# Performance work log

Measured on AMD Instinct MI355X. Metric: run time of the kernel, lower is better.

## Reference

```python
import math
import jax, jax.numpy as jnp
import numpy as np
from jax import lax

G_RATIO = 0.5       # g_ratio init arg
TMAX_RATIO = 0.25


def setup_inputs() -> dict:
    key = jax.random.key(0)
    k1, k2, k3, k4 = jax.random.split(key, 4)
    N = 4096
    cost_maps = jax.random.uniform(k1, (N,), jnp.float32)          # heuristic h(v)
    nodes = jax.random.uniform(k2, (N, 2), jnp.float32)            # coords (only size used)
    adj = (jax.random.uniform(k3, (N, N)) < 0.005).astype(jnp.float32)
    adj = jnp.maximum(adj, adj.T)                                  # symmetric PRM-like graph
    w = jax.random.uniform(k4, (N, N), jnp.float32, minval=0.1, maxval=1.0)
    weighted_adj = adj * w                                         # edge lengths
    return {"start_index": 0, "goal_index": N - 1, "cost_maps": cost_maps,
            "nodes": nodes, "adj": adj, "weighted_adj": weighted_adj}


def _astar_forward(start_index, goal_index, cost_maps, adj, weighted_adj):
    N = cost_maps.shape[0]
    inv_sqrt_n = 1.0 / math.sqrt(N)
    diag = jnp.arange(N)
    adj = adj.at[diag, diag].set(0.0)
    weighted_adj = jnp.where(jnp.isinf(weighted_adj), 0.0, weighted_adj)
    weighted_adj = weighted_adj.at[diag, diag].set(0.0)

    h = cost_maps
    goal_maps = jnp.zeros((N,), cost_maps.dtype).at[goal_index].set(1.0)
    open0 = jnp.zeros((N,), cost_maps.dtype).at[start_index].set(1.0)
    hist0 = jnp.zeros((N,), cost_maps.dtype)
    g0 = weighted_adj[start_index]
    parents0 = jnp.full((N,), float(goal_index), cost_maps.dtype)
    Tmax = int(TMAX_RATIO * N)  # training-mode budget

    def step(carry, t):
        open_m, hist, g, parents, done, t_final = carry
        f = G_RATIO * g + (1.0 - G_RATIO) * h
        f_exp = jnp.exp(-f * inv_sqrt_n) * open_m
        denom = jnp.sum(f_exp)
        y = f_exp / jnp.where(denom == 0.0, 1.0, denom)  # guard only hits after done
        ind = jnp.argmax(y)
        y_hard = jnp.zeros_like(y).at[ind].set(1.0)
        snm = lax.stop_gradient(y_hard - y) + y  # straight-through one-hot select
        solved = jnp.sum(snm * goal_maps) >= 1e-8
        open2 = jnp.clip(open_m - snm, 0.0, 1.0)
        hist2 = jnp.clip(hist + snm, 0.0, 1.0)
        neighbor = (snm @ adj) * (1.0 - open2) * (1.0 - hist2)   # row-gather via matvec
        g2 = g[ind] + weighted_adj[ind]                          # tentative g through ind
        idx = lax.stop_gradient(((1.0 - open2) * (1.0 - hist2) + open2 * (g > g2).astype(g.dtype)) * neighbor)
        g_new = lax.stop_gradient(g2 * idx + g * (1.0 - idx))
        open3 = lax.stop_gradient(jnp.clip(open2 + idx, 0.0, 1.0))
        parents_new = ind.astype(parents.dtype) * idx + parents * (1.0 - idx)
        keep = done  # freeze state after goal found (mimics torch break)
        carry_out = (jnp.where(keep, open_m, open3),
                     jnp.where(keep, hist, hist2),
                     jnp.where(keep, g, g_new),
                     jnp.where(keep, parents, parents_new),
                     done | solved,
                     jnp.where(keep, t_final, t))
        return carry_out, None

    init = (open0, hist0, g0, parents0, jnp.array(False), jnp.int32(0))
    (open_m, hist, g, parents, done, t_final), _ = lax.scan(
        step, init, jnp.arange(Tmax, dtype=jnp.int32))

    # backtrack: path_maps[loc]=1; loc=parents[loc], repeated t_final times
    parents_i = parents.astype(jnp.int32)
    path0 = goal_maps.astype(jnp.int32)
    loc0 = parents_i[goal_index]

    def bt(carry, i):
        path, loc = carry
        do = i < t_final
        path = jnp.where(do, path.at[loc].set(1), path)
        loc = jnp.where(do, parents_i[loc], loc)
        return (path, loc), None

    (path_maps, _), _ = lax.scan(bt, (path0, loc0), jnp.arange(Tmax, dtype=jnp.int32))
    return hist, path_maps


def reference(start_index, goal_index, cost_maps, nodes, adj, weighted_adj):
    # training-mode forward: returns (histories, path_maps)
    return _astar_forward(start_index, goal_index, cost_maps, adj, weighted_adj)
```

## Files before the change

### kernel.cpp

```cpp
#include <hip/hip_runtime.h>
#include <math.h>


#define NN    4096
#define TMAXI 1024
#define CAP   96
#define STR9  96

__device__ __forceinline__ float fexp_of(float g, float h, float open) {
    float f = __fadd_rn(__fmul_rn(0.5f, g), __fmul_rn(0.5f, h));
    return __fmul_rn(expf(__fmul_rn(-f, 0.015625f)), open);
}

template <int CTRL, int RMASK>
__device__ __forceinline__ double dpp_mov_d(double x) {
    int lo = __double2loint(x), hi = __double2hiint(x);
    lo = __builtin_amdgcn_update_dpp(lo, lo, CTRL, RMASK, 0xf, false);
    hi = __builtin_amdgcn_update_dpp(hi, hi, CTRL, RMASK, 0xf, false);
    return __hiloint2double(hi, lo);
}

__device__ __forceinline__ double wave_max_f64(double x) {
    x = fmax(x, dpp_mov_d<0x111, 0xf>(x));
    x = fmax(x, dpp_mov_d<0x112, 0xf>(x));
    x = fmax(x, dpp_mov_d<0x114, 0xf>(x));
    x = fmax(x, dpp_mov_d<0x118, 0xf>(x));
    x = fmax(x, dpp_mov_d<0x142, 0xa>(x));
    x = fmax(x, dpp_mov_d<0x143, 0xc>(x));
    int lo = __builtin_amdgcn_readlane(__double2loint(x), 63);
    int hi = __builtin_amdgcn_readlane(__double2hiint(x), 63);
    return __hiloint2double(hi, lo);
}

__global__ __launch_bounds__(256)
void build_csr9(const float* __restrict__ wadj, float2* __restrict__ ent)
{
    __shared__ int lcnt;
    const int r = blockIdx.x;
    if (threadIdx.x == 0) lcnt = 0;
    __syncthreads();
    const float4* wrow = (const float4*)(wadj + (size_t)r * NN);
    for (int c = 0; c < NN / (256 * 4); ++c) {
        int t4 = c * 256 + threadIdx.x;
        float4 w4 = wrow[t4];
        float wv[4] = {w4.x, w4.y, w4.z, w4.w};
        #pragma unroll
        for (int k = 0; k < 4; ++k) {
            int col = t4 * 4 + k;
            float w = wv[k];
            if (col != r && w != 0.0f && !isinf(w)) {
                int p = atomicAdd(&lcnt, 1);
                if (p < CAP)
                    ent[(size_t)r * STR9 + p] =
                        make_float2(__int_as_float(col), w);
            }
        }
    }
    __syncthreads();
    int base = min(lcnt, CAP);
    for (int p = base + (int)threadIdx.x; p < CAP; p += 256)
        ent[(size_t)r * STR9 + p] = make_float2(__int_as_float(r), 0.0f);
}

__global__ __launch_bounds__(128, 1)
void astar_fwd9(const int* __restrict__ start_p,
                const int* __restrict__ goal_p,
                const float* __restrict__ cost_maps,
                const float* __restrict__ wadj,
                const float2* __restrict__ ent,
                float* __restrict__ scratch,
                float* __restrict__ out)
{
    __shared__ __align__(16) unsigned long long ls_key[NN];
    __shared__ __align__(16) float2 ls_gp[NN];
    __shared__ __align__(16) float ls_h[NN];
    __shared__ __align__(16) unsigned long long ls_bm[64];

    const int tid = threadIdx.x;

    if (tid >= 64) {
        const float4* p = (const float4*)ent;
        const int total = NN * (STR9 / 2);
        float acc = 0.0f;
        int l = tid - 64;
        #pragma unroll 4
        for (int i = l; i < total; i += 64) acc += p[i].x;
        scratch[l] = acc;
        return;
    }

    const int lane  = tid;
    const int start = start_p[0];
    const int goal  = goal_p[0];

    {
        const float4* c4 = (const float4*)cost_maps;
        const float4* w4 = (const float4*)(wadj + (size_t)start * NN);
        const float gf = (float)goal;
        for (int c = 0; c < NN / (64 * 4); ++c) {
            int j4 = c * 64 + lane;
            float4 hv4 = c4[j4];
            float4 gv4 = w4[j4];
            if (start >= j4 * 4 && start < j4 * 4 + 4)
                ((float*)&gv4)[start - j4 * 4] = 0.0f;
            ((float4*)ls_h)[j4] = hv4;
            float gv[4] = {gv4.x, gv4.y, gv4.z, gv4.w};
            #pragma unroll
            for (int k = 0; k < 4; ++k)
                ls_gp[j4 * 4 + k] = make_float2(gv[k], gf);
        }
        for (int c = 0; c < (int)(NN * sizeof(unsigned long long) /
                                  (64 * sizeof(float4))); ++c)
            ((float4*)ls_key)[c * 64 + lane] = make_float4(0.f, 0.f, 0.f, 0.f);
        ls_bm[lane] = 0ull;
        if (lane == 0) {
            float fe = fexp_of(0.0f, ls_h[start], 1.0f);
            unsigned long long kb = 0x3FF0000000000000ull
                | ((unsigned long long)__float_as_uint(fe) << 12)
                | (unsigned)(4095 - start);
            ls_key[start] = kb;
            ls_bm[start >> 6] = kb;
        }
    }

    int ind = start;
    unsigned long long closedm = 0ull;
    int tf = 0;

    for (int t = 0; t < TMAXI; ++t) {
        const int b = ind >> 6;

        const float2* row = ent + (size_t)ind * STR9;
        float2 e0 = row[lane];
        float2 e1 = make_float2(0.0f, 0.0f);
        if (lane < 32) e1 = row[64 + lane];
        double bm_v = __longlong_as_double((long long)ls_bm[lane]);
        double kb_v = __longlong_as_double(
                          (long long)ls_key[(b << 6) + lane]);
        float  gind = ls_gp[ind].x;

        double kx = kb_v;
        if (lane == (ind & 63)) kx = 0.0;
        if (kx <= 1.0) kx = 0.0;
        double K_b = wave_max_f64(kx);

        if (lane == 0) {
            ls_key[ind] = 0x3FF0000000000000ull;
            ls_bm[b] = (unsigned long long)__double_as_longlong(K_b);
        }
        if (lane == b) closedm |= (1ull << (ind & 63));

        const float indf = (float)ind;
        double nk0 = 0.0, nk1 = 0.0;

        {
            int j = __float_as_int(e0.x);
            unsigned long long kj = ls_key[j];
            float hj = ls_h[j];
            if (kj == 0ull) {
                float g2 = __fadd_rn(gind, e0.y);
                float fe = fexp_of(g2, hj, 1.0f);
                unsigned long long kb = 0x3FF0000000000000ull
                    | ((unsigned long long)__float_as_uint(fe) << 12)
                    | (unsigned)(4095 - j);
                ls_gp[j]  = make_float2(g2, indf);
                ls_key[j] = kb;
                atomicMax(&ls_bm[j >> 6], kb);
                nk0 = __longlong_as_double((long long)kb);
            }
        }
        if (lane < 32) {
            int j = __float_as_int(e1.x);
            unsigned long long kj = ls_key[j];
            float hj = ls_h[j];
            if (kj == 0ull) {
                float g2 = __fadd_rn(gind, e1.y);
                float fe = fexp_of(g2, hj, 1.0f);
                unsigned long long kb = 0x3FF0000000000000ull
                    | ((unsigned long long)__float_as_uint(fe) << 12)
                    | (unsigned)(4095 - j);
                ls_gp[j]  = make_float2(g2, indf);
                ls_key[j] = kb;
                atomicMax(&ls_bm[j >> 6], kb);
                nk1 = __longlong_as_double((long long)kb);
            }
        }

        tf = t;
        if (ind == goal) break;

        double bmx = (lane == b) ? 0.0 : bm_v;
        double loc = fmax(fmax(bmx, kx), fmax(nk0, nk1));
        double M1 = wave_max_f64(loc);
        int ind_next;
        if (M1 > 1.0) {
            unsigned long long mb = (unsigned long long)__double_as_longlong(M1);
            ind_next = 4095 - (int)(mb & 0xFFFu);
        } else {
            ind_next = 0;
        }
        ind = __builtin_amdgcn_readfirstlane(ind_next);
    }

    ls_bm[lane] = closedm;
    for (int c = 0; c < NN / (64 * 4); ++c)
        ((float4*)ls_h)[c * 64 + lane] = make_float4(0.f, 0.f, 0.f, 0.f);
    if (lane == 0) {
        ls_h[goal] = 1.0f;
        int loc = (int)ls_gp[goal].y;
        for (int i = 0; i < tf; ++i) {
            if (ls_h[loc] != 0.0f) break;
            ls_h[loc] = 1.0f;
            loc = (int)ls_gp[loc].y;
        }
    }
    for (int c = 0; c < NN / (64 * 4); ++c) {
        int j4 = c * 64 + lane;
        unsigned long long m = ls_bm[j4 >> 4];
        unsigned int bits = (unsigned int)(m >> ((j4 & 15) * 4)) & 0xFu;
        float4 hist4;
        hist4.x = (bits & 1u) ? 1.0f : 0.0f;
        hist4.y = (bits & 2u) ? 1.0f : 0.0f;
        hist4.z = (bits & 4u) ? 1.0f : 0.0f;
        hist4.w = (bits & 8u) ? 1.0f : 0.0f;
        ((float4*)out)[j4]        = hist4;
        ((float4*)(out + NN))[j4] = ((const float4*)ls_h)[j4];
    }
}

__device__ __forceinline__ float clip01(float x) {
    return fminf(fmaxf(x, 0.0f), 1.0f);
}

__global__ __launch_bounds__(1024, 1)
void astar_fwd(const int* __restrict__ start_p,
               const int* __restrict__ goal_p,
               const float* __restrict__ cost_maps,
               const float* __restrict__ adj,
               const float* __restrict__ wadj,
               float* __restrict__ out)
{
    __shared__ __align__(16) float ls_open[NN];
    __shared__ __align__(16) float ls_hist[NN];
    __shared__ __align__(16) float ls_g[NN];
    __shared__ __align__(16) float ls_par[NN];
    __shared__ __align__(16) float ls_fe[NN];
    __shared__ __align__(16) float ls_h[NN];
    __shared__ float red_v[16];
    __shared__ float red_s[16];
    __shared__ int   red_i[16];
    __shared__ float bc_snm, bc_gind;
    __shared__ int   bc_ind, ls_done, ls_tf;

    const int tid   = threadIdx.x;
    const int start = start_p[0];
    const int goal  = goal_p[0];

    for (int k = 0; k < 4; ++k) {
        int j = tid * 4 + k;
        float hv = cost_maps[j];
        float gv = wadj[(size_t)start * NN + j];
        if (j == start) gv = 0.0f;
        float ov = (j == start) ? 1.0f : 0.0f;
        ls_h[j] = hv; ls_g[j] = gv; ls_open[j] = ov;
        ls_hist[j] = 0.0f; ls_par[j] = (float)goal;
        ls_fe[j] = fexp_of(gv, hv, ov);
    }
    if (tid == 0) { ls_done = 0; ls_tf = 0; }
    __syncthreads();

    for (int t = 0; t < TMAXI; ++t) {
        float4 fe4 = *(const float4*)&ls_fe[tid * 4];
        float v0 = fe4.x, v1 = fe4.y, v2 = fe4.z, v3 = fe4.w;
        float sum = ((v0 + v1) + v2) + v3;
        float best = v0; int bi = tid * 4;
        if (v1 > best) { best = v1; bi = tid * 4 + 1; }
        if (v2 > best) { best = v2; bi = tid * 4 + 2; }
        if (v3 > best) { best = v3; bi = tid * 4 + 3; }
        #pragma unroll
        for (int off = 32; off > 0; off >>= 1) {
            float ov = __shfl_down(best, off);
            int   oi = __shfl_down(bi, off);
            float os = __shfl_down(sum, off);
            sum += os;
            if (ov > best || (ov == best && oi < bi)) { best = ov; bi = oi; }
        }
        if ((tid & 63) == 0) {
            int w = tid >> 6;
            red_v[w] = best; red_s[w] = sum; red_i[w] = bi;
        }
        __syncthreads();
        if (tid == 0) {
            float denom = red_s[0]; best = red_v[0]; bi = red_i[0];
            #pragma unroll
            for (int w = 1; w < 16; ++w) {
                denom += red_s[w];
                if (red_v[w] > best || (red_v[w] == best && red_i[w] < bi)) {
                    best = red_v[w]; bi = red_i[w];
                }
            }
            int ind = bi;
            float dg = (denom == 0.0f) ? 1.0f : denom;
            float y_ind = ls_fe[ind] / dg;
            float snm = __fadd_rn(__fsub_rn(1.0f, y_ind), y_ind);
            ls_open[ind] = clip01(__fsub_rn(ls_open[ind], snm));
            ls_hist[ind] = clip01(__fadd_rn(ls_hist[ind], snm));
            ls_fe[ind]   = fexp_of(ls_g[ind], ls_h[ind], ls_open[ind]);
            bc_ind = ind; bc_snm = snm; bc_gind = ls_g[ind];
            ls_tf = t;
            if (ind == goal && snm >= 1e-8f) ls_done = 1;
        }
        __syncthreads();
        {
            const int   ind  = bc_ind;
            const float snm  = bc_snm;
            const float gind = bc_gind;
            const float indf = (float)ind;
            float4 a4 = ((const float4*)(adj  + (size_t)ind * NN))[tid];
            float4 w4 = ((const float4*)(wadj + (size_t)ind * NN))[tid];
            float av[4] = {a4.x, a4.y, a4.z, a4.w};
            float wvv[4] = {w4.x, w4.y, w4.z, w4.w};
            #pragma unroll
            for (int k = 0; k < 4; ++k) {
                int j = tid * 4 + k;
                float a = av[k], w = wvv[k];
                if (j == ind) { a = 0.0f; w = 0.0f; }
                if (a != 0.0f) {
                    float o = ls_open[j], hi = ls_hist[j], gj = ls_g[j];
                    float one_o = __fsub_rn(1.0f, o);
                    float one_h = __fsub_rn(1.0f, hi);
                    float sm    = __fmul_rn(snm, a);
                    float neigh = __fmul_rn(__fmul_rn(sm, one_o), one_h);
                    float g2    = __fadd_rn(gind, w);
                    float cmp   = (gj > g2) ? 1.0f : 0.0f;
                    float s   = __fadd_rn(__fmul_rn(one_o, one_h),
                                          __fmul_rn(o, cmp));
                    float idx = __fmul_rn(s, neigh);
                    if (idx != 0.0f) {
                        float omi = __fsub_rn(1.0f, idx);
                        float gn = __fadd_rn(__fmul_rn(g2, idx),
                                             __fmul_rn(gj, omi));
                        float on = clip01(__fadd_rn(o, idx));
                        float pn = __fadd_rn(__fmul_rn(indf, idx),
                                             __fmul_rn(ls_par[j], omi));
                        ls_g[j] = gn; ls_open[j] = on; ls_par[j] = pn;
                        ls_fe[j] = fexp_of(gn, ls_h[j], on);
                    }
                }
            }
        }
        __syncthreads();
        if (ls_done) break;
    }

    for (int k = 0; k < 4; ++k) {
        int j = tid * 4 + k;
        out[j] = ls_hist[j];
        out[NN + j] = (j == goal) ? 1.0f : 0.0f;
    }
    __syncthreads();
    if (tid == 0) {
        int tfv = ls_tf;
        int loc = (int)ls_par[goal];
        for (int i = 0; i < tfv; ++i) {
            out[NN + loc] = 1.0f;
            loc = (int)ls_par[loc];
        }
    }
}

extern "C" void kernel_launch(void* const* d_in, const int* in_sizes, int n_in,
                              void* d_out, int out_size, void* d_ws, size_t ws_size,
                              hipStream_t stream)
{
    const int*   start_p = (const int*)d_in[0];
    const int*   goal_p  = (const int*)d_in[1];
    const float* cost    = (const float*)d_in[2];
    const float* adj     = (const float*)d_in[4];
    const float* wadj    = (const float*)d_in[5];
    float* out = (float*)d_out;

    const size_t csr_bytes = (size_t)NN * STR9 * sizeof(float2);
    const size_t need = csr_bytes + 64 * sizeof(float);
    if (ws_size >= need) {
        float2* ent     = (float2*)d_ws;
        float*  scratch = (float*)((char*)d_ws + csr_bytes);
        build_csr9<<<dim3(NN), dim3(256), 0, stream>>>(wadj, ent);
        astar_fwd9<<<dim3(1), dim3(128), 0, stream>>>(start_p, goal_p, cost,
                                                      wadj, ent, scratch, out);
    } else {
        astar_fwd<<<dim3(1), dim3(1024), 0, stream>>>(start_p, goal_p, cost,
                                                      adj, wadj, out);
    }
}
```

Baseline: 558.4 us.

## Speculatively prefetch next node's adjacency row before neighbor expansion

Before expanding the current node's neighbors, the loop works out which node would be picked next if no new neighbor beats the existing open set, and starts loading that node's adjacency row early. On the next iteration, if the real selection matches the prediction, the preloaded row is used and the dependent global load drops off the serial critical path. A wrong guess falls back to a normal load. The cost is an extra wave reduction and an extra row load every iteration.

New measurement: 725.1 us. 1.3x slower.

```diff
diff --git a/kernel.cpp b/kernel.cpp
--- a/kernel.cpp
+++ b/kernel.cpp
@@ -127,13 +127,28 @@
     unsigned long long closedm = 0ull;
     int tf = 0;
 
+    int ind_pred = start;
+    float2 e0s, e1s = make_float2(0.0f, 0.0f);
+    {
+        const float2* prow = ent + (size_t)start * STR9;
+        e0s = prow[lane];
+        if (lane < 32) e1s = prow[64 + lane];
+    }
+
     for (int t = 0; t < TMAXI; ++t) {
         const int b = ind >> 6;
 
-        const float2* row = ent + (size_t)ind * STR9;
-        float2 e0 = row[lane];
-        float2 e1 = make_float2(0.0f, 0.0f);
-        if (lane < 32) e1 = row[64 + lane];
+        float2 e0, e1;
+        if (ind == ind_pred) {
+            e0 = e0s;
+            e1 = e1s;
+        } else {
+            const float2* row = ent + (size_t)ind * STR9;
+            e0 = row[lane];
+            e1 = make_float2(0.0f, 0.0f);
+            if (lane < 32) e1 = row[64 + lane];
+        }
+
         double bm_v = __longlong_as_double((long long)ls_bm[lane]);
         double kb_v = __longlong_as_double(
                           (long long)ls_key[(b << 6) + lane]);
@@ -149,6 +164,23 @@
             ls_bm[b] = (unsigned long long)__double_as_longlong(K_b);
         }
         if (lane == b) closedm |= (1ull << (ind & 63));
+
+        double bmx = (lane == b) ? 0.0 : bm_v;
+        {
+            double Ms = wave_max_f64(fmax(bmx, kx));
+            int ip;
+            if (Ms > 1.0) {
+                unsigned long long mbs =
+                    (unsigned long long)__double_as_longlong(Ms);
+                ip = 4095 - (int)(mbs & 0xFFFu);
+            } else {
+                ip = 0;
+            }
+            ind_pred = __builtin_amdgcn_readfirstlane(ip);
+            const float2* srow = ent + (size_t)ind_pred * STR9;
+            e0s = srow[lane];
+            if (lane < 32) e1s = srow[64 + lane];
+        }
 
         const float indf = (float)ind;
         double nk0 = 0.0, nk1 = 0.0;
@@ -189,7 +221,6 @@
         tf = t;
         if (ind == goal) break;
 
-        double bmx = (lane == b) ? 0.0 : bm_v;
         double loc = fmax(fmax(bmx, kx), fmax(nk0, nk1));
         double M1 = wave_max_f64(loc);
         int ind_next;
```

## Merge two wave reductions into one interleaved pass and prefetch next row

Applied to the files above, without the earlier changes.

Removes the separate wave-wide max for the closed block's bucket key. It is now computed together with the global argmax in one interleaved DPP reduction, and the bucket max is written after the next node is chosen. The next node's CSR row and LDS state loads move to the end of the iteration, and the neighbor key/h loads are hoisted ahead of the branches. This shortens the serial dependency chain per A* step, at the cost of more intricate bookkeeping for the bucket-max update.

Measured after the change: 568.9 us. No clear change (+1.9%).

```diff
diff --git a/kernel.cpp b/kernel.cpp
--- a/kernel.cpp
+++ b/kernel.cpp
@@ -30,6 +30,27 @@
     int lo = __builtin_amdgcn_readlane(__double2loint(x), 63);
     int hi = __builtin_amdgcn_readlane(__double2hiint(x), 63);
     return __hiloint2double(hi, lo);
+}
+
+__device__ __forceinline__ void wave_max2_f64(double& a, double& b) {
+    a = fmax(a, dpp_mov_d<0x111, 0xf>(a));
+    b = fmax(b, dpp_mov_d<0x111, 0xf>(b));
+    a = fmax(a, dpp_mov_d<0x112, 0xf>(a));
+    b = fmax(b, dpp_mov_d<0x112, 0xf>(b));
+    a = fmax(a, dpp_mov_d<0x114, 0xf>(a));
+    b = fmax(b, dpp_mov_d<0x114, 0xf>(b));
+    a = fmax(a, dpp_mov_d<0x118, 0xf>(a));
+    b = fmax(b, dpp_mov_d<0x118, 0xf>(b));
+    a = fmax(a, dpp_mov_d<0x142, 0xa>(a));
+    b = fmax(b, dpp_mov_d<0x142, 0xa>(b));
+    a = fmax(a, dpp_mov_d<0x143, 0xc>(a));
+    b = fmax(b, dpp_mov_d<0x143, 0xc>(b));
+    int alo = __builtin_amdgcn_readlane(__double2loint(a), 63);
+    int ahi = __builtin_amdgcn_readlane(__double2hiint(a), 63);
+    int blo = __builtin_amdgcn_readlane(__double2loint(b), 63);
+    int bhi = __builtin_amdgcn_readlane(__double2hiint(b), 63);
+    a = __hiloint2double(ahi, alo);
+    b = __hiloint2double(bhi, blo);
 }
 
 __global__ __launch_bounds__(256)
@@ -124,82 +145,95 @@
     }
 
     int ind = start;
+    int b   = start >> 6;
     unsigned long long closedm = 0ull;
     int tf = 0;
 
+    float2 e0, e1;
+    double bm_v, kb_v;
+    float  gind;
+    {
+        const float2* row = ent + (size_t)start * STR9;
+        e0 = row[lane];
+        e1 = make_float2(0.0f, 0.0f);
+        if (lane < 32) e1 = row[64 + lane];
+        bm_v = __longlong_as_double((long long)ls_bm[lane]);
+        kb_v = __longlong_as_double((long long)ls_key[(b << 6) + lane]);
+        gind = ls_gp[ind].x;
+    }
+
     for (int t = 0; t < TMAXI; ++t) {
-        const int b = ind >> 6;
-
-        const float2* row = ent + (size_t)ind * STR9;
-        float2 e0 = row[lane];
-        float2 e1 = make_float2(0.0f, 0.0f);
-        if (lane < 32) e1 = row[64 + lane];
-        double bm_v = __longlong_as_double((long long)ls_bm[lane]);
-        double kb_v = __longlong_as_double(
-                          (long long)ls_key[(b << 6) + lane]);
-        float  gind = ls_gp[ind].x;
-
         double kx = kb_v;
         if (lane == (ind & 63)) kx = 0.0;
         if (kx <= 1.0) kx = 0.0;
-        double K_b = wave_max_f64(kx);
-
-        if (lane == 0) {
-            ls_key[ind] = 0x3FF0000000000000ull;
-            ls_bm[b] = (unsigned long long)__double_as_longlong(K_b);
-        }
+        double bmx = (lane == b) ? 0.0 : bm_v;
+
+        if (lane == 0) ls_key[ind] = 0x3FF0000000000000ull;
         if (lane == b) closedm |= (1ull << (ind & 63));
 
         const float indf = (float)ind;
+        int j0 = __float_as_int(e0.x);
+        int j1 = __float_as_int(e1.x);
+        unsigned long long kj0 = ls_key[j0];
+        unsigned long long kj1 = ls_key[j1];
+        float hj0 = ls_h[j0];
+        float hj1 = ls_h[j1];
+
         double nk0 = 0.0, nk1 = 0.0;
 
-        {
-            int j = __float_as_int(e0.x);
-            unsigned long long kj = ls_key[j];
-            float hj = ls_h[j];
-            if (kj == 0ull) {
-                float g2 = __fadd_rn(gind, e0.y);
-                float fe = fexp_of(g2, hj, 1.0f);
-                unsigned long long kb = 0x3FF0000000000000ull
-                    | ((unsigned long long)__float_as_uint(fe) << 12)
-                    | (unsigned)(4095 - j);
-                ls_gp[j]  = make_float2(g2, indf);
-                ls_key[j] = kb;
-                atomicMax(&ls_bm[j >> 6], kb);
-                nk0 = __longlong_as_double((long long)kb);
-            }
-        }
-        if (lane < 32) {
-            int j = __float_as_int(e1.x);
-            unsigned long long kj = ls_key[j];
-            float hj = ls_h[j];
-            if (kj == 0ull) {
-                float g2 = __fadd_rn(gind, e1.y);
-                float fe = fexp_of(g2, hj, 1.0f);
-                unsigned long long kb = 0x3FF0000000000000ull
-                    | ((unsigned long long)__float_as_uint(fe) << 12)
-                    | (unsigned)(4095 - j);
-                ls_gp[j]  = make_float2(g2, indf);
-                ls_key[j] = kb;
-                atomicMax(&ls_bm[j >> 6], kb);
-                nk1 = __longlong_as_double((long long)kb);
-            }
+        if (kj0 == 0ull) {
+            float g2 = __fadd_rn(gind, e0.y);
+            float fe = fexp_of(g2, hj0, 1.0f);
+            unsigned long long kb = 0x3FF0000000000000ull
+                | ((unsigned long long)__float_as_uint(fe) << 12)
+                | (unsigned)(4095 - j0);
+            ls_gp[j0]  = make_float2(g2, indf);
+            ls_key[j0] = kb;
+            atomicMax(&ls_bm[j0 >> 6], kb);
+            nk0 = __longlong_as_double((long long)kb);
+        }
+        if (lane < 32 && kj1 == 0ull) {
+            float g2 = __fadd_rn(gind, e1.y);
+            float fe = fexp_of(g2, hj1, 1.0f);
+            unsigned long long kb = 0x3FF0000000000000ull
+                | ((unsigned long long)__float_as_uint(fe) << 12)
+                | (unsigned)(4095 - j1);
+            ls_gp[j1]  = make_float2(g2, indf);
+            ls_key[j1] = kb;
+            atomicMax(&ls_bm[j1 >> 6], kb);
+            nk1 = __longlong_as_double((long long)kb);
         }
 
         tf = t;
         if (ind == goal) break;
 
-        double bmx = (lane == b) ? 0.0 : bm_v;
-        double loc = fmax(fmax(bmx, kx), fmax(nk0, nk1));
-        double M1 = wave_max_f64(loc);
+        double cA = fmax(fmax(bmx, kx), fmax(nk0, nk1));
+        double cb0 = ((j0 >> 6) == b) ? nk0 : 0.0;
+        double cb1 = ((j1 >> 6) == b) ? nk1 : 0.0;
+        double cB = fmax(kx, fmax(cb0, cb1));
+        wave_max2_f64(cA, cB);
+
         int ind_next;
-        if (M1 > 1.0) {
-            unsigned long long mb = (unsigned long long)__double_as_longlong(M1);
+        if (cA > 1.0) {
+            unsigned long long mb = (unsigned long long)__double_as_longlong(cA);
             ind_next = 4095 - (int)(mb & 0xFFFu);
         } else {
             ind_next = 0;
         }
+        const int b_old = b;
         ind = __builtin_amdgcn_readfirstlane(ind_next);
+        b   = ind >> 6;
+
+        if (lane == 0)
+            ls_bm[b_old] = (unsigned long long)__double_as_longlong(cB);
+
+        const float2* row = ent + (size_t)ind * STR9;
+        e0 = row[lane];
+        e1 = make_float2(0.0f, 0.0f);
+        if (lane < 32) e1 = row[64 + lane];
+        bm_v = __longlong_as_double((long long)ls_bm[lane]);
+        kb_v = __longlong_as_double((long long)ls_key[(b << 6) + lane]);
+        gind = ls_gp[ind].x;
     }
 
     ls_bm[lane] = closedm;
```
